# Performance work log

Hardware: AMD Instinct MI355X
Metric: run time of the kernel (lower is better)

Reference implementation:

```python
import jax, jax.numpy as jnp
import numpy as np


def _shift(w):
    # max(0, -min(w)): scalar shift making w + shift non-negative
    return jnp.maximum(0.0, -jnp.min(w))


def shifted_linear(x, W, b=None):
    # F.linear with non-negative weights plus row-sum correction
    alpha = _shift(W)
    y = x @ (W + alpha).T - alpha * jnp.sum(x, axis=-1, keepdims=True)
    if b is not None:
        y = y + b
    return y


def shifted_depthwise_conv(x, w, b):
    # x: (B, D, L), w: (D, 1, K) depthwise; causal-style padding K-1, sliced to L by caller
    alpha = _shift(w)
    k = w.shape[2]
    pad = k - 1
    dn = ('NCH', 'OIH', 'NCH')
    groups = w.shape[0]
    y = jax.lax.conv_general_dilated(x, w + alpha, (1,), [(pad, pad)],
                                     dimension_numbers=dn, feature_group_count=groups)
    ones_k = jnp.ones_like(w)
    ssum = jax.lax.conv_general_dilated(x, ones_k, (1,), [(pad, pad)],
                                        dimension_numbers=dn, feature_group_count=groups)
    return y - alpha * ssum + b[None, :, None]


def setup_inputs() -> dict:
    key = jax.random.key(0)
    ks = jax.random.split(key, 10)
    d_model, d_inner, d_state, d_conv, dt_rank = 1024, 2048, 16, 4, 64
    B, L = 2, 1024
    s = 0.05
    return {
        'hidden_states': jax.random.normal(ks[0], (B, L, d_model), jnp.float32),
        'W_in': jax.random.normal(ks[1], (2 * d_inner, d_model), jnp.float32) * s,
        'conv_w': jax.random.normal(ks[2], (d_inner, 1, d_conv), jnp.float32) * 0.3,
        'conv_b': jax.random.normal(ks[3], (d_inner,), jnp.float32) * s,
        'W_x': jax.random.normal(ks[4], (dt_rank + 2 * d_state, d_inner), jnp.float32) * s,
        'W_dt': jax.random.normal(ks[5], (d_inner, dt_rank), jnp.float32) * s,
        'dt_bias': jax.random.normal(ks[6], (d_inner,), jnp.float32),
        'W_out': jax.random.normal(ks[7], (d_model, d_inner), jnp.float32) * s,
        'A_log': jax.random.normal(ks[8], (d_inner, d_state), jnp.float32) * 0.5,
        'D': jax.random.normal(ks[9], (d_inner,), jnp.float32),
    }


def reference(hidden_states, W_in, conv_w, conv_b, W_x, W_dt, dt_bias, W_out, A_log, D):
    b, l, dm = hidden_states.shape
    d_inner = conv_w.shape[0]
    d_state = A_log.shape[1]
    dt_rank = W_dt.shape[1]

    A = jnp.exp(A_log)  # (d_inner, d_state), always positive

    # in_proj over (b*l, d_model) -> (b, 2*d_inner, l)
    xz = shifted_linear(hidden_states.reshape(b * l, dm), W_in)
    xz = xz.reshape(b, l, 2 * d_inner).transpose(0, 2, 1)
    x, z = xz[:, :d_inner], xz[:, d_inner:]

    # depthwise shifted conv + SiLU activation, truncated to seqlen
    x = jax.nn.silu(shifted_depthwise_conv(x, conv_w, conv_b)[..., :l])

    # x_proj -> dt_raw, B, C
    x_dbl = shifted_linear(x.transpose(0, 2, 1).reshape(b * l, d_inner), W_x)
    dt_raw = x_dbl[:, :dt_rank]
    Bm = x_dbl[:, dt_rank:dt_rank + d_state].reshape(b, l, d_state).transpose(0, 2, 1)  # (b,n,l)
    Cm = x_dbl[:, dt_rank + d_state:].reshape(b, l, d_state).transpose(0, 2, 1)         # (b,n,l)
    dt = shifted_linear(dt_raw, W_dt).reshape(b, l, d_inner).transpose(0, 2, 1)          # (b,d,l)

    # delta activation (softplus) with bias, clamped
    delta = jnp.clip(jax.nn.softplus(dt + dt_bias[None, :, None]), 1e-4, 20.0)

    # global scalar shifts for B and C
    beta = _shift(Bm)
    gamma = _shift(Cm)
    B_nn = Bm + beta
    C_nn = Cm + gamma

    # precomputed per-step operands, scan axis first: (l, b, d, n)
    deltaA = jnp.exp(-jnp.einsum('bdl,dn->lbdn', delta, A))
    dBu = jnp.einsum('bdl,bnl,bdl->lbdn', delta, B_nn, x)
    C_scan = C_nn.transpose(2, 0, 1)  # (l, b, n)

    def step(xc, inp):
        dA_i, dBu_i, C_i = inp
        xc = dA_i * xc + dBu_i                                   # (b,d,n)
        y = jnp.einsum('bdn,bn->bd', xc, C_i) - gamma * jnp.sum(xc, axis=-1)
        return xc, y

    x0 = jnp.zeros((b, d_inner, d_state), dtype=delta.dtype)
    _, ys = jax.lax.scan(step, x0, (deltaA, dBu, C_scan))        # ys: (l, b, d)

    y = ys.transpose(1, 2, 0) + x * D[None, :, None]             # (b, d, l) skip term
    y = y * jax.nn.silu(z)                                       # gate activation

    out = shifted_linear(y.transpose(0, 2, 1).reshape(b * l, d_inner), W_out)
    return out.reshape(b, l, dm)
```

## Files before the change

kernel.cpp:

```cpp
#include <hip/hip_runtime.h>
#include <hip/hip_bf16.h>
#include <math.h>

#define DM 1024
#define DI 2048
#define DS 16
#define DTR 64
#define NB 2
#define LL 1024
#define TT (NB*LL)
#define SCH 16
#define NCH (LL/SCH)

typedef unsigned short u16;
typedef __attribute__((ext_vector_type(8))) short bf16x8;
typedef __attribute__((ext_vector_type(4))) float f32x4;

#define LOG2E 1.4426950408889634f

__device__ inline u16 f2bf(float f) {
  union { float f; unsigned u; } c; c.f = f;
  unsigned u = c.u;
  return (u16)((u + 0x7fffu + ((u >> 16) & 1u)) >> 16);
}
__device__ inline float bf2f(u16 u) {
  union { unsigned u; float f; } c; c.u = ((unsigned)u) << 16;
  return c.f;
}

#define GLDS16(g, l) __builtin_amdgcn_global_load_lds( \
    (const __attribute__((address_space(1))) unsigned int*)(g), \
    (__attribute__((address_space(3))) unsigned int*)(l), 16, 0, 0)

template<int BM, int BN, int EPI, int OB>
__global__ __launch_bounds__(256) void gemm_bf16(
    const u16* __restrict__ A, const u16* __restrict__ B,
    void* __restrict__ Cv, int M, int N, int K, int kpb,
    const float* __restrict__ bias) {
  constexpr int WAVES_M = BM / 64;
  constexpr int WAVES_N = 4 / WAVES_M;
  constexpr int WTM = 4;
  constexpr int WTN = BN / (WAVES_N * 16);
  constexpr int ASLABS = BM / 16;
  constexpr int SLABS = (BM + BN) / 16;
  constexpr int SPW = SLABS / 4;
  __shared__ u16 As[BM * 32];
  __shared__ u16 Bs[BN * 32];
  const int tid = threadIdx.x;
  const int wave = tid >> 6;
  const int lane = tid & 63;
  const int bm = blockIdx.y * BM;
  const int bn = blockIdx.x * BN;
  const int wm = (wave / WAVES_N) * 64;
  const int wn = (wave % WAVES_N) * (WTN * 16);
  const int r4 = lane >> 2;
  const int kc = (lane & 3) * 8;
  const int fr = lane & 15;
  const int fq = lane >> 4;
  const int koff = blockIdx.z * kpb;
  float* C = (float*)Cv + (size_t)blockIdx.z * M * N;
  u16* C16 = (u16*)Cv;

  f32x4 acc[WTM][WTN];
#pragma unroll
  for (int i = 0; i < WTM; ++i)
#pragma unroll
    for (int j = 0; j < WTN; ++j) acc[i][j] = (f32x4){0.f, 0.f, 0.f, 0.f};

  for (int k0 = koff; k0 < koff + kpb; k0 += 32) {
#pragma unroll
    for (int s = wave * SPW; s < (wave + 1) * SPW; ++s) {
      if (s < ASLABS) {
        int row = s * 16 + r4;
        GLDS16(A + (size_t)(bm + row) * K + k0 + kc, &As[s * 512]);
      } else {
        int row = (s - ASLABS) * 16 + r4;
        GLDS16(B + (size_t)(bn + row) * K + k0 + kc, &Bs[(s - ASLABS) * 512]);
      }
    }
    __syncthreads();
    bf16x8 af[WTM], bf[WTN];
#pragma unroll
    for (int i = 0; i < WTM; ++i)
      af[i] = *(const bf16x8*)&As[(wm + 16 * i + fr) * 32 + fq * 8];
#pragma unroll
    for (int j = 0; j < WTN; ++j)
      bf[j] = *(const bf16x8*)&Bs[(wn + 16 * j + fr) * 32 + fq * 8];
#pragma unroll
    for (int i = 0; i < WTM; ++i)
#pragma unroll
      for (int j = 0; j < WTN; ++j)
        acc[i][j] = __builtin_amdgcn_mfma_f32_16x16x32_bf16(af[i], bf[j], acc[i][j], 0, 0, 0);
    __syncthreads();
  }

#pragma unroll
  for (int i = 0; i < WTM; ++i) {
    int row0 = bm + wm + 16 * i + fq * 4;
#pragma unroll
    for (int j = 0; j < WTN; ++j) {
      int col = bn + wn + 16 * j + fr;
#pragma unroll
      for (int r = 0; r < 4; ++r) {
        float v = acc[i][j][r];
        if (EPI == 1) {
          v += bias[col];
          float sp = (v > 20.0f) ? v : log1pf(expf(v));
          v = fminf(fmaxf(sp, 1e-4f), 20.0f);
        }
        if (OB == 1) C16[(size_t)(row0 + r) * N + col] = f2bf(v);
        else         C[(size_t)(row0 + r) * N + col] = v;
      }
    }
  }
}

__global__ __launch_bounds__(256) void gemm3_reduce(
    const float* __restrict__ part, float* __restrict__ xdb,
    u16* __restrict__ dtraw_bf, float* __restrict__ pmin) {
  int i = blockIdx.x * 256 + threadIdx.x;
  int t = i >> 7, col = i & 127;
  float s = 0.f;
#pragma unroll
  for (int z = 0; z < 16; ++z) s += part[(size_t)z * TT * 128 + i];
  if (col < 96) xdb[t * 96 + col] = s;
  if (col < 64) dtraw_bf[t * 64 + col] = f2bf(s);
  float mn = (col >= 64 && col < 80) ? s : 3.4e38f;
#pragma unroll
  for (int o = 32; o; o >>= 1) mn = fminf(mn, __shfl_down(mn, o));
  __shared__ float sm[4];
  if ((threadIdx.x & 63) == 0) sm[threadIdx.x >> 6] = mn;
  __syncthreads();
  if (threadIdx.x == 0)
    pmin[blockIdx.x] = fminf(fminf(sm[0], sm[1]), fminf(sm[2], sm[3]));
}

__global__ __launch_bounds__(256) void beta_fin(
    const float* __restrict__ pmin, float* __restrict__ beta) {
  float mn = 3.4e38f;
#pragma unroll
  for (int k = 0; k < 4; ++k) mn = fminf(mn, pmin[threadIdx.x + 256 * k]);
#pragma unroll
  for (int o = 32; o; o >>= 1) mn = fminf(mn, __shfl_down(mn, o));
  __shared__ float sm[4];
  if ((threadIdx.x & 63) == 0) sm[threadIdx.x >> 6] = mn;
  __syncthreads();
  if (threadIdx.x == 0)
    beta[0] = fmaxf(0.0f, -fminf(fminf(sm[0], sm[1]), fminf(sm[2], sm[3])));
}

__global__ __launch_bounds__(256) void cast_all(
    const float* __restrict__ hs, const float* __restrict__ win,
    const float* __restrict__ wout, const float* __restrict__ wx,
    const float* __restrict__ wdt,
    u16* __restrict__ hs_bf, u16* __restrict__ win_bf,
    u16* __restrict__ wout_bf, u16* __restrict__ wx_bf,
    u16* __restrict__ wdt_bf) {
  int gid = blockIdx.x * 256 + threadIdx.x;
  const float* src; u16* dst; int off;
  if (gid < 524288)       { src = hs;   dst = hs_bf;   off = gid; }
  else if (gid < 1572864) { src = win;  dst = win_bf;  off = gid - 524288; }
  else if (gid < 2097152) { src = wout; dst = wout_bf; off = gid - 1572864; }
  else if (gid < 2146304) { src = wx;   dst = wx_bf;   off = gid - 2097152; }
  else if (gid < 2179072) { src = wdt;  dst = wdt_bf;  off = gid - 2146304; }
  else {
    ushort4 z4 = {0, 0, 0, 0};
    ((ushort4*)wx_bf)[49152 + gid - 2179072] = z4;
    return;
  }
  float4 v = ((const float4*)src)[off];
  ushort4 o;
  o.x = f2bf(v.x); o.y = f2bf(v.y); o.z = f2bf(v.z); o.w = f2bf(v.w);
  ((ushort4*)dst)[off] = o;
}

__global__ __launch_bounds__(256) void conv_silu4(
    const u16* __restrict__ xz, const float* __restrict__ w,
    const float* __restrict__ cb, u16* __restrict__ xc_bf) {
  int gid = blockIdx.x * 256 + threadIdx.x;
  int dq = (gid & 511) * 4;
  int t = gid >> 9;
  int l = t & (LL - 1);
  float wv[4][4];
#pragma unroll
  for (int j = 0; j < 4; ++j) {
    float4 ww = *(const float4*)&w[(dq + j) * 4];
    wv[j][0] = ww.x; wv[j][1] = ww.y; wv[j][2] = ww.z; wv[j][3] = ww.w;
  }
  float4 acc = *(const float4*)&cb[dq];
#pragma unroll
  for (int k = 0; k < 4; ++k) {
    int ll = l - 3 + k;
    if (ll < 0) continue;
    ushort4 xv = *(const ushort4*)&xz[(size_t)(t - 3 + k) * (2 * DI) + dq];
    acc.x += bf2f(xv.x) * wv[0][k]; acc.y += bf2f(xv.y) * wv[1][k];
    acc.z += bf2f(xv.z) * wv[2][k]; acc.w += bf2f(xv.w) * wv[3][k];
  }
  acc.x /= (1.0f + expf(-acc.x)); acc.y /= (1.0f + expf(-acc.y));
  acc.z /= (1.0f + expf(-acc.z)); acc.w /= (1.0f + expf(-acc.w));
  ushort4 o;
  o.x = f2bf(acc.x); o.y = f2bf(acc.y); o.z = f2bf(acc.z); o.w = f2bf(acc.w);
  *(ushort4*)&xc_bf[(size_t)t * DI + dq] = o;
}

__global__ __launch_bounds__(256) void scan_pass1(
    const float* __restrict__ delta, const u16* __restrict__ xc_bf,
    const float* __restrict__ xdb, const float* __restrict__ A_log,
    const float* __restrict__ beta_p,
    float* __restrict__ hend, float* __restrict__ Ssum) {
  const int d = blockIdx.x * 256 + threadIdx.x;
  const int c = blockIdx.y;
  const int b = blockIdx.z;
  __shared__ float Bsh[SCH][16];
  const float beta = beta_p[0];
  const int t0 = b * LL + c * SCH;
  {
    int i = threadIdx.x;
    int tt = i >> 4, n = i & 15;
    Bsh[tt][n] = xdb[(size_t)(t0 + tt) * 96 + 64 + n] + beta;
  }
  __syncthreads();
  float Av2[16];
#pragma unroll
  for (int n = 0; n < 16; ++n) Av2[n] = expf(A_log[d * 16 + n]) * LOG2E;
  float h[16];
#pragma unroll
  for (int n = 0; n < 16; ++n) h[n] = 0.f;
  float S = 0.f;
  for (int tt = 0; tt < SCH; ++tt) {
    int t = t0 + tt;
    float dv = delta[(size_t)t * DI + d];
    float xv = bf2f(xc_bf[(size_t)t * DI + d]);
    float dx = dv * xv;
    S += dv;
#pragma unroll
    for (int n = 0; n < 16; ++n) {
      float a = __builtin_amdgcn_exp2f(-dv * Av2[n]);
      h[n] = a * h[n] + dx * Bsh[tt][n];
    }
  }
  size_t base = (((size_t)(b * NCH + c) * DI) + d) * 16;
#pragma unroll
  for (int n = 0; n < 16; ++n) hend[base + n] = h[n];
  Ssum[((size_t)(b * NCH + c) * DI) + d] = S;
}

__global__ __launch_bounds__(256) void scan_pass2(
    float* __restrict__ hend, const float* __restrict__ Ssum,
    const float* __restrict__ A_log) {
  int gid = blockIdx.x * 256 + threadIdx.x;
  int n = gid & 15;
  int d = (gid >> 4) & (DI - 1);
  int b = gid >> 15;
  float Av2 = expf(A_log[d * 16 + n]) * LOG2E;
  float H = 0.f;
  for (int c = 0; c < NCH; ++c) {
    size_t cb = ((size_t)(b * NCH + c) * DI) + d;
    float hl = hend[cb * 16 + n];
    float p = __builtin_amdgcn_exp2f(-Av2 * Ssum[cb]);
    hend[cb * 16 + n] = H;
    H = p * H + hl;
  }
}

__global__ __launch_bounds__(256) void scan_pass3(
    const float* __restrict__ delta, const u16* __restrict__ xc_bf,
    const float* __restrict__ xdb, const u16* __restrict__ xz_bf,
    const float* __restrict__ A_log, const float* __restrict__ Dp,
    const float* __restrict__ beta_p, const float* __restrict__ hstart,
    u16* __restrict__ ybf) {
  const int d = blockIdx.x * 256 + threadIdx.x;
  const int c = blockIdx.y;
  const int b = blockIdx.z;
  __shared__ float Bsh[SCH][16];
  __shared__ float Csh[SCH][16];
  const float beta = beta_p[0];
  const int t0 = b * LL + c * SCH;
  {
    int i = threadIdx.x;
    int tt = i >> 4, n = i & 15;
    size_t row = (size_t)(t0 + tt) * 96;
    Bsh[tt][n] = xdb[row + 64 + n] + beta;
    Csh[tt][n] = xdb[row + 80 + n];
  }
  __syncthreads();
  float Av2[16];
#pragma unroll
  for (int n = 0; n < 16; ++n) Av2[n] = expf(A_log[d * 16 + n]) * LOG2E;
  float h[16];
  size_t base = (((size_t)(b * NCH + c) * DI) + d) * 16;
#pragma unroll
  for (int n = 0; n < 16; ++n) h[n] = hstart[base + n];
  const float Dd = Dp[d];
  for (int tt = 0; tt < SCH; ++tt) {
    int t = t0 + tt;
    float dv = delta[(size_t)t * DI + d];
    float xv = bf2f(xc_bf[(size_t)t * DI + d]);
    float dx = dv * xv;
    float yv = 0.f;
#pragma unroll
    for (int n = 0; n < 16; ++n) {
      float a = __builtin_amdgcn_exp2f(-dv * Av2[n]);
      h[n] = a * h[n] + dx * Bsh[tt][n];
      yv += h[n] * Csh[tt][n];
    }
    float zv = bf2f(xz_bf[(size_t)t * (2 * DI) + DI + d]);
    float out = (yv + xv * Dd) * (zv / (1.0f + expf(-zv)));
    ybf[(size_t)t * DI + d] = f2bf(out);
  }
}

extern "C" void kernel_launch(void* const* d_in, const int* in_sizes, int n_in,
                              void* d_out, int out_size, void* d_ws, size_t ws_size,
                              hipStream_t stream) {
  const float* hs      = (const float*)d_in[0];
  const float* W_in    = (const float*)d_in[1];
  const float* conv_w  = (const float*)d_in[2];
  const float* conv_b  = (const float*)d_in[3];
  const float* W_x     = (const float*)d_in[4];
  const float* W_dt    = (const float*)d_in[5];
  const float* dt_bias = (const float*)d_in[6];
  const float* W_out   = (const float*)d_in[7];
  const float* A_log   = (const float*)d_in[8];
  const float* Dp      = (const float*)d_in[9];
  float* out = (float*)d_out;

  float* ws      = (float*)d_ws;
  float* xz_bfR  = ws;
  float* xcv_bfR = xz_bfR + (size_t)TT * 2 * DI / 2;
  float* xdb     = xcv_bfR + (size_t)TT * DI / 2;
  float* dlt     = xdb + (size_t)TT * 96;
  float* betab   = dlt + (size_t)TT * DI;
  float* pmin    = betab + 64;
  float* hend    = pmin + 1024;
  float* Ssum    = hend + (size_t)NB * NCH * DI * 16;
  float* hs_bfR  = Ssum + (size_t)NB * NCH * DI;
  float* win_bfR = hs_bfR + (size_t)TT * DM / 2;
  float* wout_bfR = win_bfR + (size_t)2 * DI * DM / 2;
  float* wx_bfR  = wout_bfR + (size_t)DM * DI / 2;
  float* wdt_bfR = wx_bfR + 131072;
  float* dtraw_bfR = wdt_bfR + 65536;

  u16* xz_bf    = (u16*)xz_bfR;
  u16* xcv_bf   = (u16*)xcv_bfR;
  u16* hs_bf    = (u16*)hs_bfR;
  u16* win_bf   = (u16*)win_bfR;
  u16* wout_bf  = (u16*)wout_bfR;
  u16* wx_bf    = (u16*)wx_bfR;
  u16* wdt_bf   = (u16*)wdt_bfR;
  u16* dtraw_bf = (u16*)dtraw_bfR;
  u16* ybf      = (u16*)win_bfR;
  float* part   = dlt;

  dim3 blk(256);

  cast_all<<<8576, blk, 0, stream>>>(hs, W_in, W_out, W_x, W_dt,
                                     hs_bf, win_bf, wout_bf, wx_bf, wdt_bf);

  gemm_bf16<128, 128, 0, 1><<<dim3(4096 / 128, TT / 128), blk, 0, stream>>>(
      hs_bf, win_bf, xz_bf, TT, 2 * DI, DM, DM, nullptr);

  conv_silu4<<<(TT * DI / 4) / 256, blk, 0, stream>>>(xz_bf, conv_w, conv_b, xcv_bf);

  gemm_bf16<128, 128, 0, 0><<<dim3(1, TT / 128, 16), blk, 0, stream>>>(
      xcv_bf, wx_bf, part, TT, 128, DI, 128, nullptr);
  gemm3_reduce<<<(TT * 128) / 256, blk, 0, stream>>>(part, xdb, dtraw_bf, pmin);

  beta_fin<<<1, blk, 0, stream>>>(pmin, betab);

  gemm_bf16<128, 128, 1, 0><<<dim3(DI / 128, TT / 128), blk, 0, stream>>>(
      dtraw_bf, wdt_bf, dlt, TT, DI, DTR, DTR, dt_bias);

  scan_pass1<<<dim3(DI / 256, NCH, NB), blk, 0, stream>>>(
      dlt, xcv_bf, xdb, A_log, betab, hend, Ssum);
  scan_pass2<<<(NB * DI * DS) / 256, blk, 0, stream>>>(hend, Ssum, A_log);
  scan_pass3<<<dim3(DI / 256, NCH, NB), blk, 0, stream>>>(
      dlt, xcv_bf, xdb, xz_bf, A_log, Dp, betab, hend, ybf);

  gemm_bf16<64, 128, 0, 0><<<dim3(DM / 128, TT / 64), blk, 0, stream>>>(
      ybf, wout_bf, out, TT, DM, DI, DI, nullptr);
}
```

Measured before the change: 271.4 us.

## Atomic split-K for x_proj, bf16 delta, fold beta reduction into scan kernels

The split-K x_proj GEMM now accumulates its 16 partial results straight into a zeroed xdb buffer with atomic adds, instead of writing partials and running a separate reduction pass. The beta_fin kernel is dropped and each scan block recomputes the global min from the 768 partial minima. Delta is stored as bf16 instead of fp32, which halves its traffic in both scan passes. Atomic accumulation makes the sums nondeterministic, bf16 delta loses precision, and every scan block repeats the small min reduction.

```diff
diff --git a/kernel.cpp b/kernel.cpp
--- a/kernel.cpp
+++ b/kernel.cpp
@@ -11,6 +11,7 @@
 #define TT (NB*LL)
 #define SCH 16
 #define NCH (LL/SCH)
+#define NPMIN 768
 
 typedef unsigned short u16;
 typedef __attribute__((ext_vector_type(8))) short bf16x8;
@@ -58,7 +59,7 @@
   const int fr = lane & 15;
   const int fq = lane >> 4;
   const int koff = blockIdx.z * kpb;
-  float* C = (float*)Cv + (size_t)blockIdx.z * M * N;
+  float* C = (float*)Cv + (EPI == 2 ? 0 : (size_t)blockIdx.z * M * N);
   u16* C16 = (u16*)Cv;
 
   f32x4 acc[WTM][WTN];
@@ -103,27 +104,29 @@
 #pragma unroll
       for (int r = 0; r < 4; ++r) {
         float v = acc[i][j][r];
-        if (EPI == 1) {
-          v += bias[col];
-          float sp = (v > 20.0f) ? v : log1pf(expf(v));
-          v = fminf(fmaxf(sp, 1e-4f), 20.0f);
+        if (EPI == 2) {
+          if (col < 96)
+            unsafeAtomicAdd(&C[(size_t)(row0 + r) * 96 + col], v);
+        } else {
+          if (EPI == 1) {
+            v += bias[col];
+            float sp = (v > 20.0f) ? v : log1pf(expf(v));
+            v = fminf(fmaxf(sp, 1e-4f), 20.0f);
+          }
+          if (OB == 1) C16[(size_t)(row0 + r) * N + col] = f2bf(v);
+          else         C[(size_t)(row0 + r) * N + col] = v;
         }
-        if (OB == 1) C16[(size_t)(row0 + r) * N + col] = f2bf(v);
-        else         C[(size_t)(row0 + r) * N + col] = v;
       }
     }
   }
 }
 
-__global__ __launch_bounds__(256) void gemm3_reduce(
-    const float* __restrict__ part, float* __restrict__ xdb,
-    u16* __restrict__ dtraw_bf, float* __restrict__ pmin) {
+__global__ __launch_bounds__(256) void xdb_post(
+    const float* __restrict__ xdb, u16* __restrict__ dtraw_bf,
+    float* __restrict__ pmin) {
   int i = blockIdx.x * 256 + threadIdx.x;
-  int t = i >> 7, col = i & 127;
-  float s = 0.f;
-#pragma unroll
-  for (int z = 0; z < 16; ++z) s += part[(size_t)z * TT * 128 + i];
-  if (col < 96) xdb[t * 96 + col] = s;
+  int t = i / 96, col = i - t * 96;
+  float s = xdb[i];
   if (col < 64) dtraw_bf[t * 64 + col] = f2bf(s);
   float mn = (col >= 64 && col < 80) ? s : 3.4e38f;
 #pragma unroll
@@ -133,20 +136,6 @@
   __syncthreads();
   if (threadIdx.x == 0)
     pmin[blockIdx.x] = fminf(fminf(sm[0], sm[1]), fminf(sm[2], sm[3]));
-}
-
-__global__ __launch_bounds__(256) void beta_fin(
-    const float* __restrict__ pmin, float* __restrict__ beta) {
-  float mn = 3.4e38f;
-#pragma unroll
-  for (int k = 0; k < 4; ++k) mn = fminf(mn, pmin[threadIdx.x + 256 * k]);
-#pragma unroll
-  for (int o = 32; o; o >>= 1) mn = fminf(mn, __shfl_down(mn, o));
-  __shared__ float sm[4];
-  if ((threadIdx.x & 63) == 0) sm[threadIdx.x >> 6] = mn;
-  __syncthreads();
-  if (threadIdx.x == 0)
-    beta[0] = fmaxf(0.0f, -fminf(fminf(sm[0], sm[1]), fminf(sm[2], sm[3])));
 }
 
 __global__ __launch_bounds__(256) void cast_all(
@@ -155,7 +144,7 @@
     const float* __restrict__ wdt,
     u16* __restrict__ hs_bf, u16* __restrict__ win_bf,
     u16* __restrict__ wout_bf, u16* __restrict__ wx_bf,
-    u16* __restrict__ wdt_bf) {
+    u16* __restrict__ wdt_bf, float* __restrict__ xdb) {
   int gid = blockIdx.x * 256 + threadIdx.x;
   const float* src; u16* dst; int off;
   if (gid < 524288)       { src = hs;   dst = hs_bf;   off = gid; }
@@ -163,9 +152,13 @@
   else if (gid < 2097152) { src = wout; dst = wout_bf; off = gid - 1572864; }
   else if (gid < 2146304) { src = wx;   dst = wx_bf;   off = gid - 2097152; }
   else if (gid < 2179072) { src = wdt;  dst = wdt_bf;  off = gid - 2146304; }
-  else {
+  else if (gid < 2195456) {
     ushort4 z4 = {0, 0, 0, 0};
     ((ushort4*)wx_bf)[49152 + gid - 2179072] = z4;
+    return;
+  } else {
+    float4 z = {0.f, 0.f, 0.f, 0.f};
+    ((float4*)xdb)[gid - 2195456] = z;
     return;
   }
   float4 v = ((const float4*)src)[off];
@@ -203,16 +196,31 @@
   *(ushort4*)&xc_bf[(size_t)t * DI + dq] = o;
 }
 
+__device__ inline float block_beta(const float* __restrict__ pmin,
+                                   float* __restrict__ sm ) {
+  float mn = 3.4e38f;
+  for (int j = threadIdx.x; j < NPMIN; j += 256) mn = fminf(mn, pmin[j]);
+#pragma unroll
+  for (int o = 32; o; o >>= 1) mn = fminf(mn, __shfl_down(mn, o));
+  if ((threadIdx.x & 63) == 0) sm[threadIdx.x >> 6] = mn;
+  __syncthreads();
+  if (threadIdx.x == 0)
+    sm[4] = fmaxf(0.0f, -fminf(fminf(sm[0], sm[1]), fminf(sm[2], sm[3])));
+  __syncthreads();
+  return sm[4];
+}
+
 __global__ __launch_bounds__(256) void scan_pass1(
-    const float* __restrict__ delta, const u16* __restrict__ xc_bf,
+    const u16* __restrict__ dlt_bf, const u16* __restrict__ xc_bf,
     const float* __restrict__ xdb, const float* __restrict__ A_log,
-    const float* __restrict__ beta_p,
+    const float* __restrict__ pmin,
     float* __restrict__ hend, float* __restrict__ Ssum) {
   const int d = blockIdx.x * 256 + threadIdx.x;
   const int c = blockIdx.y;
   const int b = blockIdx.z;
   __shared__ float Bsh[SCH][16];
-  const float beta = beta_p[0];
+  __shared__ float smb[5];
+  const float beta = block_beta(pmin, smb);
   const int t0 = b * LL + c * SCH;
   {
     int i = threadIdx.x;
@@ -229,7 +237,7 @@
   float S = 0.f;
   for (int tt = 0; tt < SCH; ++tt) {
     int t = t0 + tt;
-    float dv = delta[(size_t)t * DI + d];
+    float dv = bf2f(dlt_bf[(size_t)t * DI + d]);
     float xv = bf2f(xc_bf[(size_t)t * DI + d]);
     float dx = dv * xv;
     S += dv;
@@ -264,17 +272,18 @@
 }
 
 __global__ __launch_bounds__(256) void scan_pass3(
-    const float* __restrict__ delta, const u16* __restrict__ xc_bf,
+    const u16* __restrict__ dlt_bf, const u16* __restrict__ xc_bf,
     const float* __restrict__ xdb, const u16* __restrict__ xz_bf,
     const float* __restrict__ A_log, const float* __restrict__ Dp,
-    const float* __restrict__ beta_p, const float* __restrict__ hstart,
+    const float* __restrict__ pmin, const float* __restrict__ hstart,
     u16* __restrict__ ybf) {
   const int d = blockIdx.x * 256 + threadIdx.x;
   const int c = blockIdx.y;
   const int b = blockIdx.z;
   __shared__ float Bsh[SCH][16];
   __shared__ float Csh[SCH][16];
-  const float beta = beta_p[0];
+  __shared__ float smb[5];
+  const float beta = block_beta(pmin, smb);
   const int t0 = b * LL + c * SCH;
   {
     int i = threadIdx.x;
@@ -294,7 +303,7 @@
   const float Dd = Dp[d];
   for (int tt = 0; tt < SCH; ++tt) {
     int t = t0 + tt;
-    float dv = delta[(size_t)t * DI + d];
+    float dv = bf2f(dlt_bf[(size_t)t * DI + d]);
     float xv = bf2f(xc_bf[(size_t)t * DI + d]);
     float dx = dv * xv;
     float yv = 0.f;
@@ -325,24 +334,24 @@
   const float* Dp      = (const float*)d_in[9];
   float* out = (float*)d_out;
 
-  float* ws      = (float*)d_ws;
-  float* xz_bfR  = ws;
-  float* xcv_bfR = xz_bfR + (size_t)TT * 2 * DI / 2;
-  float* xdb     = xcv_bfR + (size_t)TT * DI / 2;
-  float* dlt     = xdb + (size_t)TT * 96;
-  float* betab   = dlt + (size_t)TT * DI;
-  float* pmin    = betab + 64;
-  float* hend    = pmin + 1024;
-  float* Ssum    = hend + (size_t)NB * NCH * DI * 16;
-  float* hs_bfR  = Ssum + (size_t)NB * NCH * DI;
-  float* win_bfR = hs_bfR + (size_t)TT * DM / 2;
+  float* ws       = (float*)d_ws;
+  float* xz_bfR   = ws;
+  float* xcv_bfR  = xz_bfR + (size_t)TT * 2 * DI / 2;
+  float* xdb      = xcv_bfR + (size_t)TT * DI / 2;
+  float* dlt_bfR  = xdb + (size_t)TT * 96;
+  float* pmin     = dlt_bfR + (size_t)TT * DI / 2;
+  float* hend     = pmin + 1024;
+  float* Ssum     = hend + (size_t)NB * NCH * DI * 16;
+  float* hs_bfR   = Ssum + (size_t)NB * NCH * DI;
+  float* win_bfR  = hs_bfR + (size_t)TT * DM / 2;
   float* wout_bfR = win_bfR + (size_t)2 * DI * DM / 2;
-  float* wx_bfR  = wout_bfR + (size_t)DM * DI / 2;
-  float* wdt_bfR = wx_bfR + 131072;
+  float* wx_bfR   = wout_bfR + (size_t)DM * DI / 2;
+  float* wdt_bfR  = wx_bfR + 131072;
   float* dtraw_bfR = wdt_bfR + 65536;
 
   u16* xz_bf    = (u16*)xz_bfR;
   u16* xcv_bf   = (u16*)xcv_bfR;
+  u16* dlt_bf   = (u16*)dlt_bfR;
   u16* hs_bf    = (u16*)hs_bfR;
   u16* win_bf   = (u16*)win_bfR;
   u16* wout_bf  = (u16*)wout_bfR;
@@ -350,32 +359,29 @@
   u16* wdt_bf   = (u16*)wdt_bfR;
   u16* dtraw_bf = (u16*)dtraw_bfR;
   u16* ybf      = (u16*)win_bfR;
-  float* part   = dlt;
 
   dim3 blk(256);
 
-  cast_all<<<8576, blk, 0, stream>>>(hs, W_in, W_out, W_x, W_dt,
-                                     hs_bf, win_bf, wout_bf, wx_bf, wdt_bf);
+  cast_all<<<8768, blk, 0, stream>>>(hs, W_in, W_out, W_x, W_dt,
+                                     hs_bf, win_bf, wout_bf, wx_bf, wdt_bf, xdb);
 
   gemm_bf16<128, 128, 0, 1><<<dim3(4096 / 128, TT / 128), blk, 0, stream>>>(
       hs_bf, win_bf, xz_bf, TT, 2 * DI, DM, DM, nullptr);
 
   conv_silu4<<<(TT * DI / 4) / 256, blk, 0, stream>>>(xz_bf, conv_w, conv_b, xcv_bf);
 
-  gemm_bf16<128, 128, 0, 0><<<dim3(1, TT / 128, 16), blk, 0, stream>>>(
-      xcv_bf, wx_bf, part, TT, 128, DI, 128, nullptr);
-  gemm3_reduce<<<(TT * 128) / 256, blk, 0, stream>>>(part, xdb, dtraw_bf, pmin);
-
-  beta_fin<<<1, blk, 0, stream>>>(pmin, betab);
-
-  gemm_bf16<128, 128, 1, 0><<<dim3(DI / 128, TT / 128), blk, 0, stream>>>(
-      dtraw_bf, wdt_bf, dlt, TT, DI, DTR, DTR, dt_bias);
+  gemm_bf16<128, 128, 2, 0><<<dim3(1, TT / 128, 16), blk, 0, stream>>>(
+      xcv_bf, wx_bf, xdb, TT, 128, DI, 128, nullptr);
+  xdb_post<<<NPMIN, blk, 0, stream>>>(xdb, dtraw_bf, pmin);
+
+  gemm_bf16<128, 128, 1, 1><<<dim3(DI / 128, TT / 128), blk, 0, stream>>>(
+      dtraw_bf, wdt_bf, dlt_bf, TT, DI, DTR, DTR, dt_bias);
 
   scan_pass1<<<dim3(DI / 256, NCH, NB), blk, 0, stream>>>(
-      dlt, xcv_bf, xdb, A_log, betab, hend, Ssum);
+      dlt_bf, xcv_bf, xdb, A_log, pmin, hend, Ssum);
   scan_pass2<<<(NB * DI * DS) / 256, blk, 0, stream>>>(hend, Ssum, A_log);
   scan_pass3<<<dim3(DI / 256, NCH, NB), blk, 0, stream>>>(
-      dlt, xcv_bf, xdb, xz_bf, A_log, Dp, betab, hend, ybf);
+      dlt_bf, xcv_bf, xdb, xz_bf, A_log, Dp, pmin, hend, ybf);
 
   gemm_bf16<64, 128, 0, 0><<<dim3(DM / 128, TT / 64), blk, 0, stream>>>(
       ybf, wout_bf, out, TT, DM, DI, DI, nullptr);
```

After: 397.5 us. 46.4% more time.
